# Kernel tuning notes

Hardware: AMD Instinct MI355X
Metric: run time of the kernel (lower is better)

## Reference

```python
import jax, jax.numpy as jnp
import numpy as np

NC = 80
REG = 16          # DFL bins per coordinate
CONF_THRES = 0.25
IOU_THRES = 0.45
MAX_DET = 300
TOPK = 1000       # fixed-size pre-NMS candidate pool (stand-in for max_nms=30000 with A=8400)
MAX_WH = 7680.0   # class offset for class-aware NMS
LEVELS = [(80, 80, 8.0), (40, 40, 16.0), (20, 20, 32.0)]  # (h, w, stride) for imgsz=640


def _make_anchors():
    """make_anchors: grid-cell centers (+0.5 offset) and per-anchor strides."""
    pts, strs = [], []
    for h, w, s in LEVELS:
        sx = jnp.arange(w, dtype=jnp.float32) + 0.5
        sy = jnp.arange(h, dtype=jnp.float32) + 0.5
        gy, gx = jnp.meshgrid(sy, sx, indexing='ij')
        pts.append(jnp.stack([gx, gy], -1).reshape(-1, 2))
        strs.append(jnp.full((h * w,), s, dtype=jnp.float32))
    return jnp.concatenate(pts).T, jnp.concatenate(strs)  # [2, A], [A]


def _box_iou(b):  # b: [K, 4] xyxy -> [K, K] pairwise IoU
    area = (b[:, 2] - b[:, 0]) * (b[:, 3] - b[:, 1])
    lt = jnp.maximum(b[:, None, :2], b[None, :, :2])
    rb = jnp.minimum(b[:, None, 2:], b[None, :, 2:])
    wh = jnp.clip(rb - lt, 0.0)
    inter = wh[..., 0] * wh[..., 1]
    return inter / (area[:, None] + area[None, :] - inter + 1e-7)


def _nms_keep(iou, valid):
    """Greedy NMS over score-sorted candidates: keep[i] iff valid and no earlier kept box overlaps > thr."""
    K = iou.shape[0]
    idx = jnp.arange(K)
    def body(keep, i):
        sup = jnp.any((iou[i] > IOU_THRES) & keep & (idx < i))
        return keep.at[i].set(valid[i] & jnp.logical_not(sup)), None
    keep, _ = jax.lax.scan(body, jnp.zeros(K, dtype=bool), idx)
    return keep


def _forward(preds, dfl_w):
    B, C, A = preds.shape
    # DFL decode: softmax over 16 bins, expectation with arange(16) weights (the 1x1 conv)
    box_logits = preds[:, :4 * REG].reshape(B, 4, REG, A)
    dist = jnp.einsum('bqra,r->bqa', jax.nn.softmax(box_logits, axis=2), dfl_w)  # [B,4,A] ltrb
    anc, strd = _make_anchors()
    lt, rb = dist[:, :2], dist[:, 2:]
    x1y1 = anc[None] - lt
    x2y2 = anc[None] + rb
    c_xy = (x1y1 + x2y2) / 2
    wh = x2y2 - x1y1
    dbox = jnp.concatenate([c_xy, wh], axis=1) * strd  # dist2bbox(xywh) * stride, [B,4,A]
    cls = jax.nn.sigmoid(preds[:, 4 * REG:])           # [B,NC,A]
    # xywh2xyxy
    cx, cy, w, h = dbox[:, 0], dbox[:, 1], dbox[:, 2], dbox[:, 3]
    boxes = jnp.stack([cx - w / 2, cy - h / 2, cx + w / 2, cy + h / 2], axis=-1)  # [B,A,4]
    conf = jnp.max(cls, axis=1)      # [B,A]
    j = jnp.argmax(cls, axis=1)      # [B,A]
    score = jnp.where(conf > CONF_THRES, conf, -1.0)
    top_s, top_i = jax.lax.top_k(score, TOPK)                               # [B,K]
    tb = jnp.take_along_axis(boxes, top_i[..., None], axis=1)               # [B,K,4]
    tj = jnp.take_along_axis(j, top_i, axis=1)                              # [B,K]
    valid = top_s > CONF_THRES
    ob = tb + (tj.astype(preds.dtype) * MAX_WH)[..., None]                  # class-offset boxes
    iou = jax.vmap(_box_iou)(ob)                                            # [B,K,K]
    keep = jax.vmap(_nms_keep)(iou, valid)                                  # [B,K]
    sel = jnp.where(keep, top_s, -1e9)
    order = jnp.argsort(-sel, axis=1)[:, :MAX_DET]                          # kept, score-sorted
    fb = jnp.take_along_axis(tb, order[..., None], axis=1)
    fs = jnp.take_along_axis(top_s, order, axis=1)
    fj = jnp.take_along_axis(tj, order, axis=1).astype(preds.dtype)
    fv = jnp.take_along_axis(keep, order, axis=1)
    out = jnp.concatenate([fb, fs[..., None], fj[..., None]], axis=-1)
    return out * fv[..., None].astype(preds.dtype)                          # [B,300,6]


def setup_inputs() -> dict:
    key = jax.random.key(0)
    k1, _ = jax.random.split(key)
    preds = jax.random.normal(k1, (32, 4 * REG + NC, 8400), dtype=jnp.float32)
    dfl_w = jnp.arange(REG, dtype=jnp.float32)
    return {"preds": preds, "dfl_w": dfl_w}


def reference(preds, dfl_w):
    return _forward(preds, dfl_w)
```

## Files before the change

### kernel.cpp

```cpp
#include <hip/hip_runtime.h>
#include <cstdint>
#include <cstddef>

typedef unsigned long long u64;
typedef unsigned int u32;

#define A_TOT   8400
#define NCLS    80
#define KSLOT   1024
#define NCHUNK  9
#define TOPK_N  1000
#define MAXDET  300
#define OUT_STRIDE (MAXDET * 6)

#define GLOBAL_AS const __attribute__((address_space(1))) void*
#define LDS_AS __attribute__((address_space(3))) void*


__device__ __forceinline__ float sig32(float x) {
#pragma clang fp contract(off)
    float e = (float)exp(-(double)x);
    float t = 1.0f + e;
    return 1.0f / t;
}

__device__ __forceinline__ u32 key_hi_from_score(float s) {
    u32 u = __float_as_uint(s);
    return (u & 0x80000000u) ? ~u : (u | 0x80000000u);
}
__device__ __forceinline__ float score_from_key_hi(u32 t) {
    u32 u = (t & 0x80000000u) ? (t ^ 0x80000000u) : ~t;
    return __uint_as_float(u);
}

__device__ __forceinline__ u64 mp_rank(const u64* __restrict__ A,
                                       const u64* __restrict__ B, int t) {
    int lo = 0, hi = t;
    while (lo < hi) {
        int mid = (lo + hi + 1) >> 1;
        if (A[mid - 1] > B[t - mid]) lo = mid; else hi = mid - 1;
    }
    int i = lo, j = t - lo;
    u64 av = A[i], bv = B[j];
    return av > bv ? av : bv;
}

__global__ __launch_bounds__(256) void k_decode(const float* __restrict__ preds,
                                                u64* __restrict__ key_raw,
                                                float4* __restrict__ dbox) {
#pragma clang fp contract(off)
    __shared__ float tile[2][16][256];
    int b = blockIdx.y;
    int a0 = blockIdx.x * 256;
    int t = threadIdx.x;
    int a = a0 + t;
    int nA = A_TOT - a0; if (nA > 256) nA = 256;
    int p4max = nA >> 2;
    const float* pb = preds + (size_t)b * 144 * A_TOT;

    int l  = t & 63;
    int wv = t >> 6;
    int lc = (l < p4max) ? l : (p4max - 1);

    auto stage = [&](int ch0, int buf) {
#pragma unroll
        for (int k = 0; k < 4; ++k) {
            int r = 4 * k + wv;
            const float* gsrc = pb + (size_t)(ch0 + r) * A_TOT + a0 + 4 * lc;
            __builtin_amdgcn_global_load_lds((GLOBAL_AS)gsrc,
                                             (LDS_AS)&tile[buf][r][0],
                                             16, 0, 0);
        }
    };

    float d[4] = {0.f, 0.f, 0.f, 0.f};
    float m = -3.0e38f, m2 = -3.0e38f;
    int jm = 0;

    stage(0, 0);
    __syncthreads();

    for (int cb = 0; cb < 9; ++cb) {
        int buf = cb & 1;
        if (cb + 1 < 9) stage((cb + 1) * 16, (cb + 1) & 1);
        if (t < nA) {
            float x[16];
#pragma unroll
            for (int r = 0; r < 16; ++r) x[r] = tile[buf][r][t];
            if (cb < 4) {
                float mx = x[0];
#pragma unroll
                for (int r = 1; r < 16; ++r) mx = fmaxf(mx, x[r]);
                float e[16], s = 0.f;
#pragma unroll
                for (int r = 0; r < 16; ++r) { e[r] = expf(x[r] - mx); s = s + e[r]; }
                float dd = 0.f;
#pragma unroll
                for (int r = 0; r < 16; ++r) { float pr = e[r] / s; dd = dd + pr * (float)r; }
                d[cb] = dd;
            } else {
                int cbase = (cb - 4) * 16;
#pragma unroll
                for (int r = 0; r < 16; ++r) {
                    int c = cbase + r;
                    float v = x[r];
                    if (v > m) { m2 = m; m = v; jm = c; }
                    else if (v > m2) { m2 = v; }
                }
            }
        }
        if (cb < 8) __syncthreads();
    }

    if (t >= nA) return;

    const float* pc = pb + (size_t)64 * A_TOT + a;
    float conf; int cls = jm;
    if ((m - m2) < 1e-4f || m > 7.0f) {
        float sb = -1.0f; int jb = 0;
        for (int c = 0; c < NCLS; ++c) {
            float s = sig32(pc[(size_t)c * A_TOT]);
            if (s > sb) { sb = s; jb = c; }
        }
        conf = sb; cls = jb;
    } else {
        conf = sig32(m);
    }
    float score = (conf > 0.25f) ? conf : -1.0f;
    u32 hi = key_hi_from_score(score);
    u32 lo = ((0x3FFFu - (u32)a) << 7) | (u32)cls;
    key_raw[(size_t)b * A_TOT + a] = ((u64)hi << 32) | lo;

    int row, col; float stride;
    if (a < 6400)      { row = a / 80;          col = a % 80;          stride = 8.0f; }
    else if (a < 8000) { int aa = a - 6400; row = aa / 40; col = aa % 40; stride = 16.0f; }
    else               { int aa = a - 8000; row = aa / 20; col = aa % 20; stride = 32.0f; }
    float ax = (float)col + 0.5f;
    float ay = (float)row + 0.5f;
    float x1 = ax - d[0], y1 = ay - d[1];
    float x2 = ax + d[2], y2 = ay + d[3];
    float cx = (x1 + x2) / 2.0f, cy = (y1 + y2) / 2.0f;
    float w  = x2 - x1,          h  = y2 - y1;
    float4 db;
    db.x = cx * stride; db.y = cy * stride; db.z = w * stride; db.w = h * stride;
    dbox[(size_t)b * A_TOT + a] = db;
}

__global__ __launch_bounds__(1024) void k_chunksort(const u64* __restrict__ key_raw,
                                                    u64* __restrict__ key_sorted) {
    __shared__ u64 s[KSLOT];
    int b = blockIdx.y, ch = blockIdx.x, t = threadIdx.x;
    int a = ch * KSLOT + t;
    s[t] = (a < A_TOT) ? key_raw[(size_t)b * A_TOT + a] : 0ull;
    __syncthreads();
    for (int k = 2; k <= KSLOT; k <<= 1) {
        for (int j = k >> 1; j > 0; j >>= 1) {
            int ixj = t ^ j;
            if (ixj > t) {
                u64 x = s[t], y = s[ixj];
                bool descBlock = ((t & k) == 0);
                bool sw = descBlock ? (x < y) : (x > y);
                if (sw) { s[t] = y; s[ixj] = x; }
            }
            __syncthreads();
        }
    }
    key_sorted[((size_t)b * NCHUNK + ch) * KSLOT + t] = s[t];
}

__global__ __launch_bounds__(1024) void k_select(const u64* __restrict__ key_sorted,
                                                 u64* __restrict__ topk,
                                                 const float4* __restrict__ dbox,
                                                 float* __restrict__ tb,
                                                 float* __restrict__ ob,
                                                 float* __restrict__ area,
                                                 u32* __restrict__ validf) {
#pragma clang fp contract(off)
    __shared__ u64 L[5 * KSLOT];
    int b = blockIdx.x, t = threadIdx.x;
    const u64* KS = key_sorted + (size_t)b * NCHUNK * KSLOT;

    u64 r0 = mp_rank(KS + 0 * KSLOT, KS + 1 * KSLOT, t);
    u64 r1 = mp_rank(KS + 2 * KSLOT, KS + 3 * KSLOT, t);
    u64 r2 = mp_rank(KS + 4 * KSLOT, KS + 5 * KSLOT, t);
    u64 r3 = mp_rank(KS + 6 * KSLOT, KS + 7 * KSLOT, t);
    u64 r4 = KS[8 * KSLOT + t];
    L[0 * KSLOT + t] = r0; L[1 * KSLOT + t] = r1;
    L[2 * KSLOT + t] = r2; L[3 * KSLOT + t] = r3;
    L[4 * KSLOT + t] = r4;
    __syncthreads();

    u64 m0 = mp_rank(L + 0 * KSLOT, L + 1 * KSLOT, t);
    u64 m1 = mp_rank(L + 2 * KSLOT, L + 3 * KSLOT, t);
    __syncthreads();
    L[0 * KSLOT + t] = m0; L[1 * KSLOT + t] = m1;
    __syncthreads();

    u64 s0 = mp_rank(L + 0 * KSLOT, L + 1 * KSLOT, t);
    __syncthreads();
    L[0 * KSLOT + t] = s0;
    __syncthreads();

    u64 key = mp_rank(L + 0 * KSLOT, L + 4 * KSLOT, t);
    size_t si = (size_t)b * KSLOT + t;
    topk[si] = key;

    u32 hi = (u32)(key >> 32);
    u32 lo = (u32)key;
    bool valid = (t < TOPK_N) && (hi & 0x80000000u);
    if (!valid) {
        tb[si*4+0]=0.f; tb[si*4+1]=0.f; tb[si*4+2]=0.f; tb[si*4+3]=0.f;
        ob[si*4+0]=0.f; ob[si*4+1]=0.f; ob[si*4+2]=0.f; ob[si*4+3]=0.f;
        area[si] = 0.f; validf[si] = 0u;
        return;
    }
    int a   = 0x3FFF - (int)((lo >> 7) & 0x3FFFu);
    int cls = (int)(lo & 0x7Fu);

    float4 db = dbox[(size_t)b * A_TOT + a];
    float bx1 = db.x - db.z / 2.0f, by1 = db.y - db.w / 2.0f;
    float bx2 = db.x + db.z / 2.0f, by2 = db.y + db.w / 2.0f;
    tb[si*4+0] = bx1; tb[si*4+1] = by1; tb[si*4+2] = bx2; tb[si*4+3] = by2;

    float off = (float)cls * 7680.0f;
    float o0 = bx1 + off, o1 = by1 + off, o2 = bx2 + off, o3 = by2 + off;
    ob[si*4+0] = o0; ob[si*4+1] = o1; ob[si*4+2] = o2; ob[si*4+3] = o3;
    area[si] = (o2 - o0) * (o3 - o1);
    validf[si] = 1u;
}

__global__ __launch_bounds__(256) void k_matrix(const float* __restrict__ ob,
                                                const float* __restrict__ area,
                                                u64* __restrict__ masks) {
#pragma clang fp contract(off)
    __shared__ float4 sob[KSLOT];
    __shared__ float  sar[KSLOT];
    int b = blockIdx.y, rblk = blockIdx.x, tid = threadIdx.x;
    const float4* gob = (const float4*)(ob + (size_t)b * KSLOT * 4);
    const float*  gar = area + (size_t)b * KSLOT;
    for (int i = tid; i < KSLOT; i += blockDim.x) { sob[i] = gob[i]; sar[i] = gar[i]; }
    __syncthreads();

    int lane = tid & 63;
    int wave = tid >> 6;
    int i = rblk * 64 + lane;
    float4 bi = sob[i];
    float Ai = sar[i];

#pragma unroll
    for (int wl = 0; wl < 4; ++wl) {
        int w = wave * 4 + wl;
        u64 mword = 0ull;
        if (w >= rblk) {
            for (int bit = 0; bit < 64; ++bit) {
                int j = (w << 6) + bit;
                float4 bj = sob[j];
                float Aj = sar[j];
                float lt0 = fmaxf(bi.x, bj.x);
                float lt1 = fmaxf(bi.y, bj.y);
                float rb0 = fminf(bi.z, bj.z);
                float rb1 = fminf(bi.w, bj.w);
                float ww = fmaxf(rb0 - lt0, 0.0f);
                float hh = fmaxf(rb1 - lt1, 0.0f);
                float inter = ww * hh;
                float den = ((Ai + Aj) - inter) + 1e-7f;
                float iou = inter / den;
                if ((j > i) && (iou > 0.45f)) mword |= (1ull << bit);
            }
        }
        masks[((size_t)b * KSLOT + i) * 16 + w] = mword;
    }
}

__global__ __launch_bounds__(64) void k_scan(const u64* __restrict__ masks,
                                             const u32* __restrict__ validf,
                                             u64* __restrict__ keep) {
    __shared__ u64 rows[KSLOT];
    int b = blockIdx.x, lane = threadIdx.x;
    const char* base = (const char*)(masks + (size_t)b * KSLOT * 16);

    float4 r0, r1, r2, r3, r4, r5, r6, r7;
    {
        const float4* src = (const float4*)base;
        r0 = src[0*64 + lane]; r1 = src[1*64 + lane];
        r2 = src[2*64 + lane]; r3 = src[3*64 + lane];
        r4 = src[4*64 + lane]; r5 = src[5*64 + lane];
        r6 = src[6*64 + lane]; r7 = src[7*64 + lane];
    }

    u64 kw = 0ull;
    u64 rem = 0ull;
    int kept = 0;

    for (int w = 0; w < 16; ++w) {
        {
            float4* dst = (float4*)rows;
            dst[0*64 + lane] = r0; dst[1*64 + lane] = r1;
            dst[2*64 + lane] = r2; dst[3*64 + lane] = r3;
            dst[4*64 + lane] = r4; dst[5*64 + lane] = r5;
            dst[6*64 + lane] = r6; dst[7*64 + lane] = r7;
        }
        u32 vf = validf[(size_t)b * KSLOT + w * 64 + lane];
        u64 valid_w = __ballot(vf != 0u);
        __syncthreads();
        if (w < 15) {
            const float4* src = (const float4*)(base + (size_t)(w + 1) * 8192);
            r0 = src[0*64 + lane]; r1 = src[1*64 + lane];
            r2 = src[2*64 + lane]; r3 = src[3*64 + lane];
            r4 = src[4*64 + lane]; r5 = src[5*64 + lane];
            r6 = src[6*64 + lane]; r7 = src[7*64 + lane];
        }

        u64 live = valid_w & ~__shfl(rem, w);
        while (live) {
            int i = __ffsll(live) - 1;
            if (lane == w) kw |= (1ull << i);
            u64 m = (lane < 16) ? rows[i * 16 + lane] : 0ull;
            rem |= m;
            ++kept;
            if (kept >= MAXDET) break;
            live &= ~(__shfl(m, w) | (1ull << i));
        }
        if (kept >= MAXDET) break;
        __syncthreads();
    }
    if (lane < 16) keep[(size_t)b * 16 + lane] = kw;
}

__global__ __launch_bounds__(1024) void k_final(const u64* __restrict__ keep,
                                                const u64* __restrict__ topk,
                                                const float* __restrict__ tb,
                                                float* __restrict__ out) {
    __shared__ u64 kw[16];
    __shared__ int pref[16];
    int b = blockIdx.x, t = threadIdx.x;
    float* ob_ = out + (size_t)b * OUT_STRIDE;
    for (int i = t; i < OUT_STRIDE; i += blockDim.x) ob_[i] = 0.0f;
    if (t < 16) kw[t] = keep[(size_t)b * 16 + t];
    __syncthreads();
    if (t == 0) {
        int s = 0;
        for (int w = 0; w < 16; ++w) { pref[w] = s; s += __popcll(kw[w]); }
    }
    __syncthreads();
    int w = t >> 6, bit = t & 63;
    bool kp = (kw[w] >> bit) & 1ull;
    if (kp) {
        u64 below = (bit == 0) ? 0ull : (kw[w] & ((1ull << bit) - 1ull));
        int rank = pref[w] + __popcll(below);
        if (rank < MAXDET) {
            size_t si = (size_t)b * KSLOT + t;
            u64 key = topk[si];
            u32 hi = (u32)(key >> 32);
            u32 lo = (u32)key;
            float score = score_from_key_hi(hi);
            float clsf = (float)(lo & 0x7Fu);
            float* o = ob_ + rank * 6;
            o[0] = tb[si*4+0]; o[1] = tb[si*4+1];
            o[2] = tb[si*4+2]; o[3] = tb[si*4+3];
            o[4] = score; o[5] = clsf;
        }
    }
}

extern "C" void kernel_launch(void* const* d_in, const int* in_sizes, int n_in,
                              void* d_out, int out_size, void* d_ws, size_t ws_size,
                              hipStream_t stream) {
    const float* preds = (const float*)d_in[0];
    float* out = (float*)d_out;
    int B = in_sizes[0] / (144 * A_TOT);

    char* ws = (char*)d_ws;
    size_t off = 0;
    u64* key_raw    = (u64*)(ws + off); off += (size_t)B * A_TOT * 8;
    u64* key_sorted = (u64*)(ws + off); off += (size_t)B * NCHUNK * KSLOT * 8;
    u64* topk       = (u64*)(ws + off); off += (size_t)B * KSLOT * 8;
    float4* dbox    = (float4*)(ws + off); off += (size_t)B * A_TOT * 16;
    float* tb       = (float*)(ws + off); off += (size_t)B * KSLOT * 4 * 4;
    float* obuf     = (float*)(ws + off); off += (size_t)B * KSLOT * 4 * 4;
    float* area     = (float*)(ws + off); off += (size_t)B * KSLOT * 4;
    u32* validf     = (u32*)(ws + off); off += (size_t)B * KSLOT * 4;
    u64* masks      = (u64*)(ws + off); off += (size_t)B * KSLOT * 16 * 8;
    u64* keep       = (u64*)(ws + off); off += (size_t)B * 16 * 8;

    k_decode<<<dim3((A_TOT + 255) / 256, B), 256, 0, stream>>>(preds, key_raw, dbox);
    k_chunksort<<<dim3(NCHUNK, B), KSLOT, 0, stream>>>(key_raw, key_sorted);
    k_select<<<B, KSLOT, 0, stream>>>(key_sorted, topk, dbox, tb, obuf, area, validf);
    k_matrix<<<dim3(16, B), 256, 0, stream>>>(obuf, area, masks);
    k_scan<<<B, 64, 0, stream>>>(masks, validf, keep);
    k_final<<<B, 1024, 0, stream>>>(keep, topk, tb, out);
}
```

Before: 165.8 us.

## Fuse top-k select, IoU matrix, NMS scan and output into one kernel

Merges k_select, k_matrix, k_scan and k_final into a single per-image kernel that keeps boxes, areas, validity flags and the 1024x16 suppression mask in LDS. The mask table is XOR-swizzled and reuses the merge buffer through a union. Only the upper-triangular (row-block, word) pairs are enumerated across 16 waves. This removes three launches and the global round trips for the intermediate buffers. In exchange the IoU matrix for each image now runs in one 1024-thread block (32 blocks in total instead of 16x32), and the roughly 150KB of LDS allows only one block per CU.

```diff
diff --git a/kernel.cpp b/kernel.cpp
--- a/kernel.cpp
+++ b/kernel.cpp
@@ -168,94 +168,85 @@
     key_sorted[((size_t)b * NCHUNK + ch) * KSLOT + t] = s[t];
 }
 
-__global__ __launch_bounds__(1024) void k_select(const u64* __restrict__ key_sorted,
-                                                 u64* __restrict__ topk,
-                                                 const float4* __restrict__ dbox,
-                                                 float* __restrict__ tb,
-                                                 float* __restrict__ ob,
-                                                 float* __restrict__ area,
-                                                 u32* __restrict__ validf) {
+struct SNms {
+    union {
+        u64 masks[KSLOT][16];
+        u64 L[5 * KSLOT];
+    } u;
+    float4 sob[KSLOT];
+    float  sar[KSLOT];
+    u32    sval[KSLOT];
+    u64    keepw[16];
+    int    pref[16];
+};
+
+__global__ __launch_bounds__(1024) void k_nms(const u64* __restrict__ key_sorted,
+                                              const float4* __restrict__ dbox,
+                                              float* __restrict__ out) {
 #pragma clang fp contract(off)
-    __shared__ u64 L[5 * KSLOT];
+    __shared__ SNms sm;
     int b = blockIdx.x, t = threadIdx.x;
     const u64* KS = key_sorted + (size_t)b * NCHUNK * KSLOT;
+    u64* Lp = sm.u.L;
 
     u64 r0 = mp_rank(KS + 0 * KSLOT, KS + 1 * KSLOT, t);
     u64 r1 = mp_rank(KS + 2 * KSLOT, KS + 3 * KSLOT, t);
     u64 r2 = mp_rank(KS + 4 * KSLOT, KS + 5 * KSLOT, t);
     u64 r3 = mp_rank(KS + 6 * KSLOT, KS + 7 * KSLOT, t);
     u64 r4 = KS[8 * KSLOT + t];
-    L[0 * KSLOT + t] = r0; L[1 * KSLOT + t] = r1;
-    L[2 * KSLOT + t] = r2; L[3 * KSLOT + t] = r3;
-    L[4 * KSLOT + t] = r4;
-    __syncthreads();
-
-    u64 m0 = mp_rank(L + 0 * KSLOT, L + 1 * KSLOT, t);
-    u64 m1 = mp_rank(L + 2 * KSLOT, L + 3 * KSLOT, t);
-    __syncthreads();
-    L[0 * KSLOT + t] = m0; L[1 * KSLOT + t] = m1;
-    __syncthreads();
-
-    u64 s0 = mp_rank(L + 0 * KSLOT, L + 1 * KSLOT, t);
-    __syncthreads();
-    L[0 * KSLOT + t] = s0;
-    __syncthreads();
-
-    u64 key = mp_rank(L + 0 * KSLOT, L + 4 * KSLOT, t);
-    size_t si = (size_t)b * KSLOT + t;
-    topk[si] = key;
+    Lp[0 * KSLOT + t] = r0; Lp[1 * KSLOT + t] = r1;
+    Lp[2 * KSLOT + t] = r2; Lp[3 * KSLOT + t] = r3;
+    Lp[4 * KSLOT + t] = r4;
+    __syncthreads();
+    u64 m0 = mp_rank(Lp + 0 * KSLOT, Lp + 1 * KSLOT, t);
+    u64 m1 = mp_rank(Lp + 2 * KSLOT, Lp + 3 * KSLOT, t);
+    __syncthreads();
+    Lp[0 * KSLOT + t] = m0; Lp[1 * KSLOT + t] = m1;
+    __syncthreads();
+    u64 s0 = mp_rank(Lp + 0 * KSLOT, Lp + 1 * KSLOT, t);
+    __syncthreads();
+    Lp[0 * KSLOT + t] = s0;
+    __syncthreads();
+    u64 key = mp_rank(Lp + 0 * KSLOT, Lp + 4 * KSLOT, t);
 
     u32 hi = (u32)(key >> 32);
     u32 lo = (u32)key;
     bool valid = (t < TOPK_N) && (hi & 0x80000000u);
+    float bx1 = 0.f, by1 = 0.f, bx2 = 0.f, by2 = 0.f;
     if (!valid) {
-        tb[si*4+0]=0.f; tb[si*4+1]=0.f; tb[si*4+2]=0.f; tb[si*4+3]=0.f;
-        ob[si*4+0]=0.f; ob[si*4+1]=0.f; ob[si*4+2]=0.f; ob[si*4+3]=0.f;
-        area[si] = 0.f; validf[si] = 0u;
-        return;
-    }
-    int a   = 0x3FFF - (int)((lo >> 7) & 0x3FFFu);
-    int cls = (int)(lo & 0x7Fu);
-
-    float4 db = dbox[(size_t)b * A_TOT + a];
-    float bx1 = db.x - db.z / 2.0f, by1 = db.y - db.w / 2.0f;
-    float bx2 = db.x + db.z / 2.0f, by2 = db.y + db.w / 2.0f;
-    tb[si*4+0] = bx1; tb[si*4+1] = by1; tb[si*4+2] = bx2; tb[si*4+3] = by2;
-
-    float off = (float)cls * 7680.0f;
-    float o0 = bx1 + off, o1 = by1 + off, o2 = bx2 + off, o3 = by2 + off;
-    ob[si*4+0] = o0; ob[si*4+1] = o1; ob[si*4+2] = o2; ob[si*4+3] = o3;
-    area[si] = (o2 - o0) * (o3 - o1);
-    validf[si] = 1u;
-}
-
-__global__ __launch_bounds__(256) void k_matrix(const float* __restrict__ ob,
-                                                const float* __restrict__ area,
-                                                u64* __restrict__ masks) {
-#pragma clang fp contract(off)
-    __shared__ float4 sob[KSLOT];
-    __shared__ float  sar[KSLOT];
-    int b = blockIdx.y, rblk = blockIdx.x, tid = threadIdx.x;
-    const float4* gob = (const float4*)(ob + (size_t)b * KSLOT * 4);
-    const float*  gar = area + (size_t)b * KSLOT;
-    for (int i = tid; i < KSLOT; i += blockDim.x) { sob[i] = gob[i]; sar[i] = gar[i]; }
-    __syncthreads();
-
-    int lane = tid & 63;
-    int wave = tid >> 6;
-    int i = rblk * 64 + lane;
-    float4 bi = sob[i];
-    float Ai = sar[i];
-
-#pragma unroll
-    for (int wl = 0; wl < 4; ++wl) {
-        int w = wave * 4 + wl;
-        u64 mword = 0ull;
-        if (w >= rblk) {
+        sm.sob[t] = make_float4(0.f, 0.f, 0.f, 0.f);
+        sm.sar[t] = 0.f; sm.sval[t] = 0u;
+    } else {
+        int a   = 0x3FFF - (int)((lo >> 7) & 0x3FFFu);
+        int cls = (int)(lo & 0x7Fu);
+        float4 db = dbox[(size_t)b * A_TOT + a];
+        bx1 = db.x - db.z / 2.0f; by1 = db.y - db.w / 2.0f;
+        bx2 = db.x + db.z / 2.0f; by2 = db.y + db.w / 2.0f;
+        float off = (float)cls * 7680.0f;
+        float o0 = bx1 + off, o1 = by1 + off, o2 = bx2 + off, o3 = by2 + off;
+        sm.sob[t] = make_float4(o0, o1, o2, o3);
+        sm.sar[t] = (o2 - o0) * (o3 - o1);
+        sm.sval[t] = 1u;
+    }
+    __syncthreads();
+
+    for (int z = t; z < KSLOT * 16; z += 1024) ((u64*)sm.u.masks)[z] = 0ull;
+    __syncthreads();
+
+    {
+        int lane = t & 63, wv = t >> 6;
+        for (int p = wv; p < 136; p += 16) {
+            int rblk = 0, acc = 0;
+            while (acc + (16 - rblk) <= p) { acc += 16 - rblk; ++rblk; }
+            int w = rblk + (p - acc);
+            int i = rblk * 64 + lane;
+            float4 bi = sm.sob[i];
+            float Ai = sm.sar[i];
+            u64 mword = 0ull;
             for (int bit = 0; bit < 64; ++bit) {
                 int j = (w << 6) + bit;
-                float4 bj = sob[j];
-                float Aj = sar[j];
+                float4 bj = sm.sob[j];
+                float Aj = sm.sar[j];
                 float lt0 = fmaxf(bi.x, bj.x);
                 float lt1 = fmaxf(bi.y, bj.y);
                 float rb0 = fminf(bi.z, bj.z);
@@ -267,97 +258,51 @@
                 float iou = inter / den;
                 if ((j > i) && (iou > 0.45f)) mword |= (1ull << bit);
             }
-        }
-        masks[((size_t)b * KSLOT + i) * 16 + w] = mword;
-    }
-}
-
-__global__ __launch_bounds__(64) void k_scan(const u64* __restrict__ masks,
-                                             const u32* __restrict__ validf,
-                                             u64* __restrict__ keep) {
-    __shared__ u64 rows[KSLOT];
-    int b = blockIdx.x, lane = threadIdx.x;
-    const char* base = (const char*)(masks + (size_t)b * KSLOT * 16);
-
-    float4 r0, r1, r2, r3, r4, r5, r6, r7;
-    {
-        const float4* src = (const float4*)base;
-        r0 = src[0*64 + lane]; r1 = src[1*64 + lane];
-        r2 = src[2*64 + lane]; r3 = src[3*64 + lane];
-        r4 = src[4*64 + lane]; r5 = src[5*64 + lane];
-        r6 = src[6*64 + lane]; r7 = src[7*64 + lane];
-    }
-
-    u64 kw = 0ull;
-    u64 rem = 0ull;
-    int kept = 0;
-
-    for (int w = 0; w < 16; ++w) {
-        {
-            float4* dst = (float4*)rows;
-            dst[0*64 + lane] = r0; dst[1*64 + lane] = r1;
-            dst[2*64 + lane] = r2; dst[3*64 + lane] = r3;
-            dst[4*64 + lane] = r4; dst[5*64 + lane] = r5;
-            dst[6*64 + lane] = r6; dst[7*64 + lane] = r7;
-        }
-        u32 vf = validf[(size_t)b * KSLOT + w * 64 + lane];
-        u64 valid_w = __ballot(vf != 0u);
-        __syncthreads();
-        if (w < 15) {
-            const float4* src = (const float4*)(base + (size_t)(w + 1) * 8192);
-            r0 = src[0*64 + lane]; r1 = src[1*64 + lane];
-            r2 = src[2*64 + lane]; r3 = src[3*64 + lane];
-            r4 = src[4*64 + lane]; r5 = src[5*64 + lane];
-            r6 = src[6*64 + lane]; r7 = src[7*64 + lane];
-        }
-
-        u64 live = valid_w & ~__shfl(rem, w);
-        while (live) {
-            int i = __ffsll(live) - 1;
-            if (lane == w) kw |= (1ull << i);
-            u64 m = (lane < 16) ? rows[i * 16 + lane] : 0ull;
-            rem |= m;
-            ++kept;
+            sm.u.masks[i][w ^ (i & 7)] = mword;
+        }
+    }
+    __syncthreads();
+
+    if (t < 64) {
+        int lane = t;
+        u64 kw = 0ull, rem = 0ull;
+        int kept = 0;
+        for (int cw = 0; cw < 16; ++cw) {
+            u32 vf = sm.sval[cw * 64 + lane];
+            u64 valid_w = __ballot(vf != 0u);
+            u64 live = valid_w & ~__shfl(rem, cw);
+            while (live) {
+                int i = __ffsll(live) - 1;
+                if (lane == cw) kw |= (1ull << i);
+                int rowi = cw * 64 + i;
+                u64 mm = (lane < 16) ? sm.u.masks[rowi][lane ^ (rowi & 7)] : 0ull;
+                rem |= mm;
+                ++kept;
+                if (kept >= MAXDET) break;
+                live &= ~(__shfl(mm, cw) | (1ull << i));
+            }
             if (kept >= MAXDET) break;
-            live &= ~(__shfl(m, w) | (1ull << i));
-        }
-        if (kept >= MAXDET) break;
-        __syncthreads();
-    }
-    if (lane < 16) keep[(size_t)b * 16 + lane] = kw;
-}
-
-__global__ __launch_bounds__(1024) void k_final(const u64* __restrict__ keep,
-                                                const u64* __restrict__ topk,
-                                                const float* __restrict__ tb,
-                                                float* __restrict__ out) {
-    __shared__ u64 kw[16];
-    __shared__ int pref[16];
-    int b = blockIdx.x, t = threadIdx.x;
-    float* ob_ = out + (size_t)b * OUT_STRIDE;
-    for (int i = t; i < OUT_STRIDE; i += blockDim.x) ob_[i] = 0.0f;
-    if (t < 16) kw[t] = keep[(size_t)b * 16 + t];
-    __syncthreads();
+        }
+        if (lane < 16) sm.keepw[lane] = kw;
+    }
+    __syncthreads();
+
+    float* outb = out + (size_t)b * OUT_STRIDE;
+    for (int z = t; z < OUT_STRIDE; z += 1024) outb[z] = 0.0f;
     if (t == 0) {
-        int s = 0;
-        for (int w = 0; w < 16; ++w) { pref[w] = s; s += __popcll(kw[w]); }
-    }
-    __syncthreads();
-    int w = t >> 6, bit = t & 63;
-    bool kp = (kw[w] >> bit) & 1ull;
-    if (kp) {
-        u64 below = (bit == 0) ? 0ull : (kw[w] & ((1ull << bit) - 1ull));
-        int rank = pref[w] + __popcll(below);
+        int s2 = 0;
+        for (int w2 = 0; w2 < 16; ++w2) { sm.pref[w2] = s2; s2 += __popcll(sm.keepw[w2]); }
+    }
+    __syncthreads();
+    int w3 = t >> 6, bit3 = t & 63;
+    if ((sm.keepw[w3] >> bit3) & 1ull) {
+        u64 below = (bit3 == 0) ? 0ull : (sm.keepw[w3] & ((1ull << bit3) - 1ull));
+        int rank = sm.pref[w3] + __popcll(below);
         if (rank < MAXDET) {
-            size_t si = (size_t)b * KSLOT + t;
-            u64 key = topk[si];
-            u32 hi = (u32)(key >> 32);
-            u32 lo = (u32)key;
             float score = score_from_key_hi(hi);
             float clsf = (float)(lo & 0x7Fu);
-            float* o = ob_ + rank * 6;
-            o[0] = tb[si*4+0]; o[1] = tb[si*4+1];
-            o[2] = tb[si*4+2]; o[3] = tb[si*4+3];
+            float* o = outb + rank * 6;
+            o[0] = bx1; o[1] = by1; o[2] = bx2; o[3] = by2;
             o[4] = score; o[5] = clsf;
         }
     }
@@ -374,19 +319,9 @@
     size_t off = 0;
     u64* key_raw    = (u64*)(ws + off); off += (size_t)B * A_TOT * 8;
     u64* key_sorted = (u64*)(ws + off); off += (size_t)B * NCHUNK * KSLOT * 8;
-    u64* topk       = (u64*)(ws + off); off += (size_t)B * KSLOT * 8;
     float4* dbox    = (float4*)(ws + off); off += (size_t)B * A_TOT * 16;
-    float* tb       = (float*)(ws + off); off += (size_t)B * KSLOT * 4 * 4;
-    float* obuf     = (float*)(ws + off); off += (size_t)B * KSLOT * 4 * 4;
-    float* area     = (float*)(ws + off); off += (size_t)B * KSLOT * 4;
-    u32* validf     = (u32*)(ws + off); off += (size_t)B * KSLOT * 4;
-    u64* masks      = (u64*)(ws + off); off += (size_t)B * KSLOT * 16 * 8;
-    u64* keep       = (u64*)(ws + off); off += (size_t)B * 16 * 8;
 
     k_decode<<<dim3((A_TOT + 255) / 256, B), 256, 0, stream>>>(preds, key_raw, dbox);
     k_chunksort<<<dim3(NCHUNK, B), KSLOT, 0, stream>>>(key_raw, key_sorted);
-    k_select<<<B, KSLOT, 0, stream>>>(key_sorted, topk, dbox, tb, obuf, area, validf);
-    k_matrix<<<dim3(16, B), 256, 0, stream>>>(obuf, area, masks);
-    k_scan<<<B, 64, 0, stream>>>(masks, validf, keep);
-    k_final<<<B, 1024, 0, stream>>>(keep, topk, tb, out);
-}
+    k_nms<<<B, KSLOT, 0, stream>>>(key_sorted, dbox, out);
+}
```

Measured after the change: 241.8 us. 45.8% more time.

## Stage merge inputs in LDS, prefetch NMS rows, fuse final gather into scan

Applied to the files above, without the earlier changes.

k_select now copies all nine sorted chunks into shared memory first, so the first merge round's binary searches hit LDS instead of global memory. The greedy NMS scan prefetches the next candidate's mask row speculatively, taking the LDS load off the serial dependency chain. The separate k_final kernel is folded into k_scan, removing one launch and the keep-mask round trip through global memory. In exchange, output writing and zeroing now run on a single 64-thread wave per batch instead of 1024 threads, and k_select needs a larger shared-memory buffer.

```diff
diff --git a/kernel.cpp b/kernel.cpp
--- a/kernel.cpp
+++ b/kernel.cpp
@@ -33,8 +33,7 @@
     return __uint_as_float(u);
 }
 
-__device__ __forceinline__ u64 mp_rank(const u64* __restrict__ A,
-                                       const u64* __restrict__ B, int t) {
+__device__ __forceinline__ u64 mp_rank(const u64* A, const u64* B, int t) {
     int lo = 0, hi = t;
     while (lo < hi) {
         int mid = (lo + hi + 1) >> 1;
@@ -176,32 +175,35 @@
                                                  float* __restrict__ area,
                                                  u32* __restrict__ validf) {
 #pragma clang fp contract(off)
-    __shared__ u64 L[5 * KSLOT];
+    __shared__ u64 CH[NCHUNK * KSLOT];
     int b = blockIdx.x, t = threadIdx.x;
     const u64* KS = key_sorted + (size_t)b * NCHUNK * KSLOT;
-
-    u64 r0 = mp_rank(KS + 0 * KSLOT, KS + 1 * KSLOT, t);
-    u64 r1 = mp_rank(KS + 2 * KSLOT, KS + 3 * KSLOT, t);
-    u64 r2 = mp_rank(KS + 4 * KSLOT, KS + 5 * KSLOT, t);
-    u64 r3 = mp_rank(KS + 6 * KSLOT, KS + 7 * KSLOT, t);
-    u64 r4 = KS[8 * KSLOT + t];
-    L[0 * KSLOT + t] = r0; L[1 * KSLOT + t] = r1;
-    L[2 * KSLOT + t] = r2; L[3 * KSLOT + t] = r3;
-    L[4 * KSLOT + t] = r4;
-    __syncthreads();
-
-    u64 m0 = mp_rank(L + 0 * KSLOT, L + 1 * KSLOT, t);
-    u64 m1 = mp_rank(L + 2 * KSLOT, L + 3 * KSLOT, t);
-    __syncthreads();
-    L[0 * KSLOT + t] = m0; L[1 * KSLOT + t] = m1;
-    __syncthreads();
-
-    u64 s0 = mp_rank(L + 0 * KSLOT, L + 1 * KSLOT, t);
-    __syncthreads();
-    L[0 * KSLOT + t] = s0;
-    __syncthreads();
-
-    u64 key = mp_rank(L + 0 * KSLOT, L + 4 * KSLOT, t);
+    for (int idx = t; idx < NCHUNK * KSLOT; idx += 1024) CH[idx] = KS[idx];
+    __syncthreads();
+
+    u64 r0 = mp_rank(CH + 0 * KSLOT, CH + 1 * KSLOT, t);
+    u64 r1 = mp_rank(CH + 2 * KSLOT, CH + 3 * KSLOT, t);
+    u64 r2 = mp_rank(CH + 4 * KSLOT, CH + 5 * KSLOT, t);
+    u64 r3 = mp_rank(CH + 6 * KSLOT, CH + 7 * KSLOT, t);
+    u64 r4 = CH[8 * KSLOT + t];
+    __syncthreads();
+    CH[0 * KSLOT + t] = r0; CH[1 * KSLOT + t] = r1;
+    CH[2 * KSLOT + t] = r2; CH[3 * KSLOT + t] = r3;
+    CH[4 * KSLOT + t] = r4;
+    __syncthreads();
+
+    u64 m0 = mp_rank(CH + 0 * KSLOT, CH + 1 * KSLOT, t);
+    u64 m1 = mp_rank(CH + 2 * KSLOT, CH + 3 * KSLOT, t);
+    __syncthreads();
+    CH[0 * KSLOT + t] = m0; CH[1 * KSLOT + t] = m1;
+    __syncthreads();
+
+    u64 s0 = mp_rank(CH + 0 * KSLOT, CH + 1 * KSLOT, t);
+    __syncthreads();
+    CH[0 * KSLOT + t] = s0;
+    __syncthreads();
+
+    u64 key = mp_rank(CH + 0 * KSLOT, CH + 4 * KSLOT, t);
     size_t si = (size_t)b * KSLOT + t;
     topk[si] = key;
 
@@ -274,8 +276,12 @@
 
 __global__ __launch_bounds__(64) void k_scan(const u64* __restrict__ masks,
                                              const u32* __restrict__ validf,
-                                             u64* __restrict__ keep) {
+                                             const u64* __restrict__ topk,
+                                             const float* __restrict__ tb,
+                                             float* __restrict__ out) {
     __shared__ u64 rows[KSLOT];
+    __shared__ u64 keepw[16];
+    __shared__ int pref[16];
     int b = blockIdx.x, lane = threadIdx.x;
     const char* base = (const char*)(masks + (size_t)b * KSLOT * 16);
 
@@ -292,7 +298,7 @@
     u64 rem = 0ull;
     int kept = 0;
 
-    for (int w = 0; w < 16; ++w) {
+    for (int cw = 0; cw < 16; ++cw) {
         {
             float4* dst = (float4*)rows;
             dst[0*64 + lane] = r0; dst[1*64 + lane] = r1;
@@ -300,65 +306,69 @@
             dst[4*64 + lane] = r4; dst[5*64 + lane] = r5;
             dst[6*64 + lane] = r6; dst[7*64 + lane] = r7;
         }
-        u32 vf = validf[(size_t)b * KSLOT + w * 64 + lane];
+        u32 vf = validf[(size_t)b * KSLOT + cw * 64 + lane];
         u64 valid_w = __ballot(vf != 0u);
         __syncthreads();
-        if (w < 15) {
-            const float4* src = (const float4*)(base + (size_t)(w + 1) * 8192);
+        if (cw < 15) {
+            const float4* src = (const float4*)(base + (size_t)(cw + 1) * 8192);
             r0 = src[0*64 + lane]; r1 = src[1*64 + lane];
             r2 = src[2*64 + lane]; r3 = src[3*64 + lane];
             r4 = src[4*64 + lane]; r5 = src[5*64 + lane];
             r6 = src[6*64 + lane]; r7 = src[7*64 + lane];
         }
 
-        u64 live = valid_w & ~__shfl(rem, w);
-        while (live) {
+        u64 live = valid_w & ~__shfl(rem, cw);
+        if (live) {
             int i = __ffsll(live) - 1;
-            if (lane == w) kw |= (1ull << i);
             u64 m = (lane < 16) ? rows[i * 16 + lane] : 0ull;
-            rem |= m;
-            ++kept;
-            if (kept >= MAXDET) break;
-            live &= ~(__shfl(m, w) | (1ull << i));
+            for (;;) {
+                if (lane == cw) kw |= (1ull << i);
+                rem |= m;
+                ++kept;
+                if (kept >= MAXDET) break;
+                u64 live_wo = live & ~(1ull << i);
+                int g = -1; u64 mg = 0ull;
+                if (live_wo) {
+                    g = __ffsll(live_wo) - 1;
+                    mg = (lane < 16) ? rows[g * 16 + lane] : 0ull;
+                }
+                live = live_wo & ~__shfl(m, cw);
+                if (!live) break;
+                i = __ffsll(live) - 1;
+                m = (i == g) ? mg : ((lane < 16) ? rows[i * 16 + lane] : 0ull);
+            }
         }
         if (kept >= MAXDET) break;
         __syncthreads();
     }
-    if (lane < 16) keep[(size_t)b * 16 + lane] = kw;
-}
-
-__global__ __launch_bounds__(1024) void k_final(const u64* __restrict__ keep,
-                                                const u64* __restrict__ topk,
-                                                const float* __restrict__ tb,
-                                                float* __restrict__ out) {
-    __shared__ u64 kw[16];
-    __shared__ int pref[16];
-    int b = blockIdx.x, t = threadIdx.x;
-    float* ob_ = out + (size_t)b * OUT_STRIDE;
-    for (int i = t; i < OUT_STRIDE; i += blockDim.x) ob_[i] = 0.0f;
-    if (t < 16) kw[t] = keep[(size_t)b * 16 + t];
-    __syncthreads();
-    if (t == 0) {
+
+    if (lane < 16) keepw[lane] = kw;
+    __syncthreads();
+    if (lane == 0) {
         int s = 0;
-        for (int w = 0; w < 16; ++w) { pref[w] = s; s += __popcll(kw[w]); }
-    }
-    __syncthreads();
-    int w = t >> 6, bit = t & 63;
-    bool kp = (kw[w] >> bit) & 1ull;
-    if (kp) {
-        u64 below = (bit == 0) ? 0ull : (kw[w] & ((1ull << bit) - 1ull));
-        int rank = pref[w] + __popcll(below);
-        if (rank < MAXDET) {
-            size_t si = (size_t)b * KSLOT + t;
-            u64 key = topk[si];
-            u32 hi = (u32)(key >> 32);
-            u32 lo = (u32)key;
-            float score = score_from_key_hi(hi);
-            float clsf = (float)(lo & 0x7Fu);
-            float* o = ob_ + rank * 6;
-            o[0] = tb[si*4+0]; o[1] = tb[si*4+1];
-            o[2] = tb[si*4+2]; o[3] = tb[si*4+3];
-            o[4] = score; o[5] = clsf;
+        for (int w = 0; w < 16; ++w) { pref[w] = s; s += __popcll(keepw[w]); }
+    }
+    __syncthreads();
+    float* outb = out + (size_t)b * OUT_STRIDE;
+    for (int z = lane; z < OUT_STRIDE; z += 64) outb[z] = 0.0f;
+    __syncthreads();
+    for (int w2 = 0; w2 < 16; ++w2) {
+        u64 kwv = keepw[w2];
+        if ((kwv >> lane) & 1ull) {
+            u64 below = (lane == 0) ? 0ull : (kwv & ((1ull << lane) - 1ull));
+            int rank = pref[w2] + __popcll(below);
+            if (rank < MAXDET) {
+                size_t si = (size_t)b * KSLOT + w2 * 64 + lane;
+                u64 key = topk[si];
+                u32 hi = (u32)(key >> 32);
+                u32 lo = (u32)key;
+                float score = score_from_key_hi(hi);
+                float clsf = (float)(lo & 0x7Fu);
+                float* o = outb + rank * 6;
+                o[0] = tb[si*4+0]; o[1] = tb[si*4+1];
+                o[2] = tb[si*4+2]; o[3] = tb[si*4+3];
+                o[4] = score; o[5] = clsf;
+            }
         }
     }
 }
@@ -381,12 +391,10 @@
     float* area     = (float*)(ws + off); off += (size_t)B * KSLOT * 4;
     u32* validf     = (u32*)(ws + off); off += (size_t)B * KSLOT * 4;
     u64* masks      = (u64*)(ws + off); off += (size_t)B * KSLOT * 16 * 8;
-    u64* keep       = (u64*)(ws + off); off += (size_t)B * 16 * 8;
 
     k_decode<<<dim3((A_TOT + 255) / 256, B), 256, 0, stream>>>(preds, key_raw, dbox);
     k_chunksort<<<dim3(NCHUNK, B), KSLOT, 0, stream>>>(key_raw, key_sorted);
     k_select<<<B, KSLOT, 0, stream>>>(key_sorted, topk, dbox, tb, obuf, area, validf);
     k_matrix<<<dim3(16, B), 256, 0, stream>>>(obuf, area, masks);
-    k_scan<<<B, 64, 0, stream>>>(masks, validf, keep);
-    k_final<<<B, 1024, 0, stream>>>(keep, topk, tb, out);
-}
+    k_scan<<<B, 64, 0, stream>>>(masks, validf, topk, tb, out);
+}
```

New measurement: 181.8 us. +9.6%, slower.

## Fuse NMS scan and final gather, transpose mask layout, pipeline greedy scan

Applied to the files above, without the earlier changes.

Stores the IoU suppression masks transposed (word-major) and merges the greedy scan kernel with the final output kernel into one 1024-thread block per image. The whole mask matrix is loaded into LDS up front. The serial scan prefetches the next candidate's mask rows to hide LDS latency. This removes a kernel launch and the keep-buffer round trip, at the cost of about 128KB of LDS per block and a single-wave serial section inside a large block.

```diff
diff --git a/kernel.cpp b/kernel.cpp
--- a/kernel.cpp
+++ b/kernel.cpp
@@ -33,8 +33,7 @@
     return __uint_as_float(u);
 }
 
-__device__ __forceinline__ u64 mp_rank(const u64* __restrict__ A,
-                                       const u64* __restrict__ B, int t) {
+__device__ __forceinline__ u64 mp_rank(const u64* A, const u64* B, int t) {
     int lo = 0, hi = t;
     while (lo < hi) {
         int mid = (lo + hi + 1) >> 1;
@@ -231,7 +230,7 @@
 
 __global__ __launch_bounds__(256) void k_matrix(const float* __restrict__ ob,
                                                 const float* __restrict__ area,
-                                                u64* __restrict__ masks) {
+                                                u64* __restrict__ masksT) {
 #pragma clang fp contract(off)
     __shared__ float4 sob[KSLOT];
     __shared__ float  sar[KSLOT];
@@ -268,86 +267,87 @@
                 if ((j > i) && (iou > 0.45f)) mword |= (1ull << bit);
             }
         }
-        masks[((size_t)b * KSLOT + i) * 16 + w] = mword;
-    }
-}
-
-__global__ __launch_bounds__(64) void k_scan(const u64* __restrict__ masks,
-                                             const u32* __restrict__ validf,
-                                             u64* __restrict__ keep) {
-    __shared__ u64 rows[KSLOT];
-    int b = blockIdx.x, lane = threadIdx.x;
-    const char* base = (const char*)(masks + (size_t)b * KSLOT * 16);
-
-    float4 r0, r1, r2, r3, r4, r5, r6, r7;
-    {
-        const float4* src = (const float4*)base;
-        r0 = src[0*64 + lane]; r1 = src[1*64 + lane];
-        r2 = src[2*64 + lane]; r3 = src[3*64 + lane];
-        r4 = src[4*64 + lane]; r5 = src[5*64 + lane];
-        r6 = src[6*64 + lane]; r7 = src[7*64 + lane];
-    }
-
-    u64 kw = 0ull;
-    u64 rem = 0ull;
-    int kept = 0;
-
-    for (int w = 0; w < 16; ++w) {
-        {
-            float4* dst = (float4*)rows;
-            dst[0*64 + lane] = r0; dst[1*64 + lane] = r1;
-            dst[2*64 + lane] = r2; dst[3*64 + lane] = r3;
-            dst[4*64 + lane] = r4; dst[5*64 + lane] = r5;
-            dst[6*64 + lane] = r6; dst[7*64 + lane] = r7;
-        }
-        u32 vf = validf[(size_t)b * KSLOT + w * 64 + lane];
-        u64 valid_w = __ballot(vf != 0u);
-        __syncthreads();
-        if (w < 15) {
-            const float4* src = (const float4*)(base + (size_t)(w + 1) * 8192);
-            r0 = src[0*64 + lane]; r1 = src[1*64 + lane];
-            r2 = src[2*64 + lane]; r3 = src[3*64 + lane];
-            r4 = src[4*64 + lane]; r5 = src[5*64 + lane];
-            r6 = src[6*64 + lane]; r7 = src[7*64 + lane];
-        }
-
-        u64 live = valid_w & ~__shfl(rem, w);
-        while (live) {
-            int i = __ffsll(live) - 1;
-            if (lane == w) kw |= (1ull << i);
-            u64 m = (lane < 16) ? rows[i * 16 + lane] : 0ull;
-            rem |= m;
-            ++kept;
-            if (kept >= MAXDET) break;
-            live &= ~(__shfl(m, w) | (1ull << i));
-        }
-        if (kept >= MAXDET) break;
-        __syncthreads();
-    }
-    if (lane < 16) keep[(size_t)b * 16 + lane] = kw;
-}
-
-__global__ __launch_bounds__(1024) void k_final(const u64* __restrict__ keep,
-                                                const u64* __restrict__ topk,
-                                                const float* __restrict__ tb,
-                                                float* __restrict__ out) {
-    __shared__ u64 kw[16];
+        masksT[((size_t)b * 16 + w) * KSLOT + i] = mword;
+    }
+}
+
+__global__ __launch_bounds__(1024) void k_scan(const u64* __restrict__ masksT,
+                                               const u32* __restrict__ validf,
+                                               const u64* __restrict__ topk,
+                                               const float* __restrict__ tb,
+                                               float* __restrict__ out) {
+    __shared__ u64 MT[16][KSLOT + 1];
+    __shared__ u64 validw[16];
+    __shared__ u64 keepw[16];
     __shared__ int pref[16];
     int b = blockIdx.x, t = threadIdx.x;
-    float* ob_ = out + (size_t)b * OUT_STRIDE;
-    for (int i = t; i < OUT_STRIDE; i += blockDim.x) ob_[i] = 0.0f;
-    if (t < 16) kw[t] = keep[(size_t)b * 16 + t];
-    __syncthreads();
+    int lane = t & 63, wv = t >> 6;
+
+    const u64* src = masksT + (size_t)b * 16 * KSLOT;
+    for (int it = 0; it < 16; ++it)
+        MT[it][t] = src[it * KSLOT + t];
+    {
+        u32 vf = validf[(size_t)b * KSLOT + wv * 64 + lane];
+        u64 bal = __ballot(vf != 0u);
+        if (lane == 0) validw[wv] = bal;
+    }
+    __syncthreads();
+
+    if (wv == 0) {
+        u64 rem = 0ull;
+        int kept = 0;
+        for (int cw = 0; cw < 16; ++cw) {
+            u64 kw = 0ull;
+            u64 live = validw[cw] & ~__shfl(rem, cw);
+            if (live) {
+                int i1 = __ffsll(live) - 1;
+                int ri1 = cw * 64 + i1;
+                u64 mA = MT[cw][ri1];
+                u64 rA = (lane < 16) ? MT[lane][ri1] : 0ull;
+                for (;;) {
+                    kw |= (1ull << i1);
+                    rem |= rA;
+                    ++kept;
+                    if (kept >= MAXDET) break;
+                    u64 live2 = live & ~(1ull << i1);
+                    if (!live2) break;
+                    int i2 = __ffsll(live2) - 1;
+                    int ri2 = cw * 64 + i2;
+                    u64 mB = MT[cw][ri2];
+                    u64 rB = (lane < 16) ? MT[lane][ri2] : 0ull;
+                    live = live2 & ~mA;
+                    if (!live) break;
+                    int inext = __ffsll(live) - 1;
+                    if (inext == i2) { i1 = i2; mA = mB; rA = rB; }
+                    else {
+                        i1 = inext;
+                        int ri3 = cw * 64 + i1;
+                        mA = MT[cw][ri3];
+                        rA = (lane < 16) ? MT[lane][ri3] : 0ull;
+                    }
+                }
+            }
+            if (lane == 0) keepw[cw] = kw;
+            if (kept >= MAXDET) {
+                if (lane == 0)
+                    for (int w2 = cw + 1; w2 < 16; ++w2) keepw[w2] = 0ull;
+                break;
+            }
+        }
+    }
+    __syncthreads();
+
+    float* outb = out + (size_t)b * OUT_STRIDE;
+    for (int z = t; z < OUT_STRIDE; z += 1024) outb[z] = 0.0f;
     if (t == 0) {
         int s = 0;
-        for (int w = 0; w < 16; ++w) { pref[w] = s; s += __popcll(kw[w]); }
-    }
-    __syncthreads();
-    int w = t >> 6, bit = t & 63;
-    bool kp = (kw[w] >> bit) & 1ull;
-    if (kp) {
-        u64 below = (bit == 0) ? 0ull : (kw[w] & ((1ull << bit) - 1ull));
-        int rank = pref[w] + __popcll(below);
+        for (int w = 0; w < 16; ++w) { pref[w] = s; s += __popcll(keepw[w]); }
+    }
+    __syncthreads();
+    int w3 = t >> 6, bit3 = t & 63;
+    if ((keepw[w3] >> bit3) & 1ull) {
+        u64 below = (bit3 == 0) ? 0ull : (keepw[w3] & ((1ull << bit3) - 1ull));
+        int rank = pref[w3] + __popcll(below);
         if (rank < MAXDET) {
             size_t si = (size_t)b * KSLOT + t;
             u64 key = topk[si];
@@ -355,7 +355,7 @@
             u32 lo = (u32)key;
             float score = score_from_key_hi(hi);
             float clsf = (float)(lo & 0x7Fu);
-            float* o = ob_ + rank * 6;
+            float* o = outb + rank * 6;
             o[0] = tb[si*4+0]; o[1] = tb[si*4+1];
             o[2] = tb[si*4+2]; o[3] = tb[si*4+3];
             o[4] = score; o[5] = clsf;
@@ -380,13 +380,11 @@
     float* obuf     = (float*)(ws + off); off += (size_t)B * KSLOT * 4 * 4;
     float* area     = (float*)(ws + off); off += (size_t)B * KSLOT * 4;
     u32* validf     = (u32*)(ws + off); off += (size_t)B * KSLOT * 4;
-    u64* masks      = (u64*)(ws + off); off += (size_t)B * KSLOT * 16 * 8;
-    u64* keep       = (u64*)(ws + off); off += (size_t)B * 16 * 8;
+    u64* masksT     = (u64*)(ws + off); off += (size_t)B * 16 * KSLOT * 8;
 
     k_decode<<<dim3((A_TOT + 255) / 256, B), 256, 0, stream>>>(preds, key_raw, dbox);
     k_chunksort<<<dim3(NCHUNK, B), KSLOT, 0, stream>>>(key_raw, key_sorted);
     k_select<<<B, KSLOT, 0, stream>>>(key_sorted, topk, dbox, tb, obuf, area, validf);
-    k_matrix<<<dim3(16, B), 256, 0, stream>>>(obuf, area, masks);
-    k_scan<<<B, 64, 0, stream>>>(masks, validf, keep);
-    k_final<<<B, 1024, 0, stream>>>(keep, topk, tb, out);
-}
+    k_matrix<<<dim3(16, B), 256, 0, stream>>>(obuf, area, masksT);
+    k_scan<<<B, KSLOT, 0, stream>>>(masksT, validf, topk, tb, out);
+}
```

Result: slower. 177.0 us (+6.7%).
